# Performance work log

Hardware: AMD Instinct MI355X
Metric: run time of the kernel (lower is better)

## Reference

```python
import jax, jax.numpy as jnp
import numpy as np

DIM = 8          # per-head dim
EPS = 1e-15
GROUPS_PW = 192  # 3 * heads = 3 * 64


def _conv(x, w, groups=1, pad=0):
    return jax.lax.conv_general_dilated(
        x, w, window_strides=(1, 1), padding=[(pad, pad), (pad, pad)],
        dimension_numbers=('NCHW', 'OIHW', 'NCHW'), feature_group_count=groups)


def setup_inputs() -> dict:
    key = jax.random.key(0)
    k0, k1, k2, k3, k4 = jax.random.split(key, 5)
    B, C, H, W = 4, 512, 64, 64
    td = 512  # heads * dim
    x = jax.random.normal(k0, (B, C, H, W), jnp.float32)
    w_qkv = jax.random.normal(k1, (3 * td, C, 1, 1), jnp.float32) * 0.05
    w_dw = jax.random.normal(k2, (3 * td, 1, 5, 5), jnp.float32) * 0.05
    w_pw = jax.random.normal(k3, (3 * td, (3 * td) // GROUPS_PW, 1, 1), jnp.float32) * 0.05
    w_proj = jax.random.normal(k4, (C, 2 * td, 1, 1), jnp.float32) * 0.05
    return {'x': x, 'w_qkv': w_qkv, 'w_dw': w_dw, 'w_pw': w_pw, 'w_proj': w_proj}


def reference(x, w_qkv, w_dw, w_pw, w_proj):
    # qkv projection (1x1 conv, no bias, no norm/act per config)
    qkv = _conv(x, w_qkv)  # [B, 3*td, H, W]
    # multi-scale aggregation: depthwise 5x5 then grouped 1x1 (groups = 3*heads)
    agg = _conv(_conv(qkv, w_dw, groups=w_dw.shape[0], pad=2), w_pw, groups=GROUPS_PW)
    qkv = jnp.concatenate([qkv, agg], axis=1)  # [B, 6*td, H, W]

    B, _, H, W = qkv.shape
    qkv = qkv.reshape(B, -1, 3 * DIM, H * W)  # [B, h_eff, 3*dim, HW]
    q = jax.nn.relu(qkv[:, :, :DIM])          # [B, h, dim, HW]
    k = jax.nn.relu(qkv[:, :, DIM:2 * DIM])   # [B, h, dim, HW]
    v = qkv[:, :, 2 * DIM:]                   # [B, h, dim, HW]
    # pad v with a row of ones -> normalization trick
    v = jnp.pad(v, ((0, 0), (0, 0), (0, 1), (0, 0)), constant_values=1.0)
    # linear attention via associativity: (v k^T) q
    vk = jnp.einsum('bhdn,bhen->bhde', v, k)   # [B, h, dim+1, dim]
    out = jnp.einsum('bhde,bhen->bhdn', vk, q) # [B, h, dim+1, HW]
    out = out[:, :, :-1] / (out[:, :, -1:] + EPS)
    out = out.reshape(B, -1, H, W)             # [B, 2*td, H, W]
    return x + _conv(out, w_proj)
```

## Files before the change

kernel.cpp:

```cpp
#include <hip/hip_runtime.h>
#include <hip/hip_bf16.h>
#include <cstdint>
#include <cstddef>


typedef __hip_bfloat16 bf16;
typedef __attribute__((ext_vector_type(8))) short short8;
typedef __attribute__((ext_vector_type(4))) float f32x4;

__device__ __forceinline__ float b2f(bf16 v) { return __bfloat162float(v); }
__device__ __forceinline__ bf16 f2b(float v) { return __float2bfloat16(v); }

__device__ __forceinline__ void async16(void* lds_base, const void* gaddr) {
    __builtin_amdgcn_global_load_lds(
        (const __attribute__((address_space(1))) unsigned int*)gaddr,
        (__attribute__((address_space(3))) unsigned int*)lds_base,
        16, 0, 0);
}

__global__ __launch_bounds__(256) void convert_kernel(
    const float* __restrict__ src, bf16* __restrict__ dst, int n)
{
    int i = blockIdx.x * 256 + threadIdx.x;
    if (i < n) dst[i] = f2b(src[i]);
}

__global__ __launch_bounds__(256) void transpose_x_kernel(
    const float* __restrict__ x, bf16* __restrict__ x_t)
{
    __shared__ bf16 tile[32][33];
    const int b = blockIdx.z;
    const int c0 = blockIdx.y * 32;
    const int n0 = blockIdx.x * 32;
    const int tx = threadIdx.x & 31, ty = threadIdx.x >> 5;
    #pragma unroll
    for (int i = 0; i < 32; i += 8)
        tile[ty + i][tx] = f2b(x[((size_t)b * 512 + c0 + ty + i) * 4096 + n0 + tx]);
    __syncthreads();
    #pragma unroll
    for (int i = 0; i < 32; i += 8)
        x_t[((size_t)b * 4096 + n0 + ty + i) * 512 + c0 + tx] = tile[tx][ty + i];
}

template <bool PROJ>
__global__ __launch_bounds__(256) void mfma_gemm_kernel(
    const bf16* __restrict__ A, const bf16* __restrict__ xt_or_qkv,
    const bf16* __restrict__ agg, const float* __restrict__ X,
    void* __restrict__ Cout, int M, int K)
{
    constexpr int N = 4096;
    const int b = blockIdx.z;
    const int m_blk = blockIdx.y * 128;
    const int n_blk = blockIdx.x * 128;

    __shared__ short As[128 * 32];
    __shared__ short Bs[128 * 32];

    const int tid = threadIdx.x;
    const int lane = tid & 63, wave = tid >> 6;
    const int wm = (wave >> 1) * 64, wn = (wave & 1) * 64;
    const int fm = lane & 15, fq = lane >> 4;

    f32x4 acc[4][4] = {};

    const short* Ag = (const short*)A;
    const short* Btg = PROJ ? nullptr
        : (const short*)(xt_or_qkv + (size_t)b * N * 512);

    for (int k0 = 0; k0 < K; k0 += 32) {
        #pragma unroll
        for (int t0 = 0; t0 < 2; ++t0) {
            int t = wave + t0 * 4;
            int row = m_blk + t * 16 + (lane >> 2);
            int col = k0 + (lane & 3) * 8;
            async16(&As[t * 512], Ag + (size_t)row * K + col);
        }
        #pragma unroll
        for (int t0 = 0; t0 < 2; ++t0) {
            int t = wave + t0 * 4;
            int n = n_blk + t * 16 + (lane >> 2);
            if (!PROJ) {
                int col = k0 + (lane & 3) * 8;
                async16(&Bs[t * 512], Btg + (size_t)n * 512 + col);
            } else {
                int h = (k0 >> 3) + (lane & 3);
                const bf16* chunk = (h < 64 ? xt_or_qkv : agg) +
                    ((size_t)b * 1536 + (size_t)(h & 63) * 24 + 16) * 4096;
                async16(&Bs[t * 512], chunk + (size_t)n * 8);
            }
        }
        __syncthreads();

        short8 af[4], bfv[4];
        #pragma unroll
        for (int i = 0; i < 4; ++i)
            af[i] = *(const short8*)&As[(wm + i * 16 + fm) * 32 + fq * 8];
        #pragma unroll
        for (int j = 0; j < 4; ++j)
            bfv[j] = *(const short8*)&Bs[(wn + j * 16 + fm) * 32 + fq * 8];
        #pragma unroll
        for (int i = 0; i < 4; ++i)
            #pragma unroll
            for (int j = 0; j < 4; ++j)
                acc[i][j] = __builtin_amdgcn_mfma_f32_16x16x32_bf16(
                    af[i], bfv[j], acc[i][j], 0, 0, 0);
        __syncthreads();
    }

    if (!PROJ) {
        bf16* Cb = (bf16*)Cout + (size_t)b * M * N;
        #pragma unroll
        for (int i = 0; i < 4; ++i)
            #pragma unroll
            for (int j = 0; j < 4; ++j) {
                int n = n_blk + wn + j * 16 + fm;
                #pragma unroll
                for (int r = 0; r < 4; ++r) {
                    int m = m_blk + wm + i * 16 + fq * 4 + r;
                    Cb[(size_t)m * N + n] = f2b(acc[i][j][r]);
                }
            }
    } else {
        float* Ob = (float*)Cout + (size_t)b * M * N;
        const float* Xb = X + (size_t)b * M * N;
        #pragma unroll
        for (int i = 0; i < 4; ++i)
            #pragma unroll
            for (int j = 0; j < 4; ++j) {
                int n = n_blk + wn + j * 16 + fm;
                #pragma unroll
                for (int r = 0; r < 4; ++r) {
                    int m = m_blk + wm + i * 16 + fq * 4 + r;
                    size_t off = (size_t)m * N + n;
                    Ob[off] = acc[i][j][r] + Xb[off];
                }
            }
    }
}

__global__ __launch_bounds__(256) void dwpw_kernel(
    const bf16* __restrict__ qkv, const float* __restrict__ w_dw,
    const float* __restrict__ w_pw, bf16* __restrict__ agg)
{
    const int bg = blockIdx.y;
    const int b = bg / 192;
    const int g = bg - b * 192;
    const int y0 = blockIdx.x * 32;

    __shared__ float s_wdw[8][28];
    __shared__ float s_wpw[8][8];

    const int tid = threadIdx.x;

    if (tid < 200) {
        int c = tid / 25, k = tid - c * 25;
        s_wdw[c][k] = w_dw[(size_t)(g * 8 + c) * 25 + k];
    }
    if (tid < 64)
        s_wpw[tid >> 3][tid & 7] = w_pw[(size_t)(g * 8 + (tid >> 3)) * 8 + (tid & 7)];
    __syncthreads();

    const int py = tid >> 3;
    const int sx = tid & 7;
    const int yq = y0 + py;
    const size_t chan_base = ((size_t)b * 1536 + g * 8) * 4096;

    const int lo_off = (sx > 0) ? 16 * sx - 4 : 0;
    const int hi_off = (sx < 7) ? 16 * sx + 16 : 0;
    const unsigned lo_keep = (sx > 0) ? 0xFFFFFFFFu : 0u;
    const unsigned hi_keep = (sx < 7) ? 0xFFFFFFFFu : 0u;

    float dwv[8][8];
    #pragma unroll
    for (int c = 0; c < 8; ++c) {
        float w[25];
        #pragma unroll
        for (int q = 0; q < 6; ++q)
            *(float4*)&w[q * 4] = *(const float4*)&s_wdw[c][q * 4];
        w[24] = s_wdw[c][24];

        const char* cbase = (const char*)(qkv + chan_base + (size_t)c * 4096);
        float a[8] = {};
        #pragma unroll
        for (int i = 0; i < 5; ++i) {
            const int y = yq + i - 2;
            const bool row_ok = ((unsigned)y < 64u);
            const int yc = row_ok ? y : 0;
            const char* rowp = cbase + yc * 128;
            uint4 mid = *(const uint4*)(rowp + 16 * sx);
            unsigned lo = *(const unsigned*)(rowp + lo_off);
            unsigned hi = *(const unsigned*)(rowp + hi_off);
            const unsigned m = row_ok ? 0xFFFFFFFFu : 0u;
            lo &= m & lo_keep;
            hi &= m & hi_keep;
            mid.x &= m; mid.y &= m; mid.z &= m; mid.w &= m;

            float f[12];
            f[0]  = __uint_as_float(lo << 16);
            f[1]  = __uint_as_float(lo & 0xFFFF0000u);
            f[2]  = __uint_as_float(mid.x << 16);
            f[3]  = __uint_as_float(mid.x & 0xFFFF0000u);
            f[4]  = __uint_as_float(mid.y << 16);
            f[5]  = __uint_as_float(mid.y & 0xFFFF0000u);
            f[6]  = __uint_as_float(mid.z << 16);
            f[7]  = __uint_as_float(mid.z & 0xFFFF0000u);
            f[8]  = __uint_as_float(mid.w << 16);
            f[9]  = __uint_as_float(mid.w & 0xFFFF0000u);
            f[10] = __uint_as_float(hi << 16);
            f[11] = __uint_as_float(hi & 0xFFFF0000u);

            #pragma unroll
            for (int j = 0; j < 5; ++j) {
                float wi = w[i * 5 + j];
                #pragma unroll
                for (int x = 0; x < 8; ++x) a[x] += f[j + x] * wi;
            }
        }
        #pragma unroll
        for (int x = 0; x < 8; ++x) dwv[c][x] = a[x];
    }

    const size_t out_pix = (size_t)yq * 64 + 8 * sx;
    #pragma unroll
    for (int o = 0; o < 8; ++o) {
        float wv[8];
        *(float4*)&wv[0] = *(const float4*)&s_wpw[o][0];
        *(float4*)&wv[4] = *(const float4*)&s_wpw[o][4];
        float s[8] = {};
        #pragma unroll
        for (int i = 0; i < 8; ++i)
            #pragma unroll
            for (int x = 0; x < 8; ++x) s[x] += dwv[i][x] * wv[i];
        union { bf16 hv[8]; uint4 u; } pk;
        #pragma unroll
        for (int x = 0; x < 8; ++x) pk.hv[x] = f2b(s[x]);
        *(uint4*)(agg + chan_base + (size_t)o * 4096 + out_pix) = pk.u;
    }
}

__global__ __launch_bounds__(256) void vk_kernel(
    const bf16* __restrict__ qkv, const bf16* __restrict__ agg,
    float* __restrict__ vk)
{
    const int bh = blockIdx.x;
    const int b = bh >> 7;
    const int h = bh & 127;
    const bf16* base = (h < 64)
        ? (qkv + ((size_t)b * 1536 + h * 24) * 4096)
        : (agg + ((size_t)b * 1536 + (h - 64) * 24) * 4096);

    const int tid = threadIdx.x;
    float acc[9][8] = {};

    for (int n = tid; n < 4096; n += 256) {
        float kv[8], vv[8];
        #pragma unroll
        for (int e = 0; e < 8; ++e) kv[e] = fmaxf(b2f(base[(size_t)(8 + e) * 4096 + n]), 0.f);
        #pragma unroll
        for (int d = 0; d < 8; ++d) vv[d] = b2f(base[(size_t)(16 + d) * 4096 + n]);
        #pragma unroll
        for (int d = 0; d < 8; ++d)
            #pragma unroll
            for (int e = 0; e < 8; ++e)
                acc[d][e] += vv[d] * kv[e];
        #pragma unroll
        for (int e = 0; e < 8; ++e) acc[8][e] += kv[e];
    }

    __shared__ float red[4][72];
    const int lane = tid & 63, wave = tid >> 6;
    #pragma unroll
    for (int d = 0; d < 9; ++d) {
        #pragma unroll
        for (int e = 0; e < 8; ++e) {
            float v = acc[d][e];
            #pragma unroll
            for (int off = 32; off > 0; off >>= 1) v += __shfl_down(v, off, 64);
            if (lane == 0) red[wave][d * 8 + e] = v;
        }
    }
    __syncthreads();
    if (tid < 72) {
        float v = red[0][tid] + red[1][tid] + red[2][tid] + red[3][tid];
        vk[(size_t)bh * 72 + tid] = v;
    }
}

__global__ __launch_bounds__(256) void attn_out_kernel(
    bf16* __restrict__ qkv, bf16* __restrict__ agg,
    const float* __restrict__ vk)
{
    const int b = blockIdx.z;
    const int h = blockIdx.y;
    const int n = blockIdx.x * 256 + threadIdx.x;
    bf16* base = (h < 64)
        ? (qkv + ((size_t)b * 1536 + h * 24) * 4096)
        : (agg + ((size_t)b * 1536 + (h - 64) * 24) * 4096);

    __shared__ float s_vk[72];
    if (threadIdx.x < 72)
        s_vk[threadIdx.x] = vk[((size_t)b * 128 + h) * 72 + threadIdx.x];
    __syncthreads();

    float q[8];
    #pragma unroll
    for (int e = 0; e < 8; ++e) q[e] = fmaxf(b2f(base[(size_t)e * 4096 + n]), 0.f);

    float o[9];
    #pragma unroll
    for (int d = 0; d < 9; ++d) {
        float s = 0.f;
        #pragma unroll
        for (int e = 0; e < 8; ++e) s += s_vk[d * 8 + e] * q[e];
        o[d] = s;
    }
    const float denom = o[8] + 1e-15f;

    union { bf16 hv[8]; uint4 u; } pk;
    #pragma unroll
    for (int d = 0; d < 8; ++d) pk.hv[d] = f2b(o[d] / denom);
    *(uint4*)((char*)(base + (size_t)16 * 4096) + (size_t)n * 16) = pk.u;
}

extern "C" void kernel_launch(void* const* d_in, const int* in_sizes, int n_in,
                              void* d_out, int out_size, void* d_ws, size_t ws_size,
                              hipStream_t stream) {
    const float* x      = (const float*)d_in[0];
    const float* w_qkv  = (const float*)d_in[1];
    const float* w_dw   = (const float*)d_in[2];
    const float* w_pw   = (const float*)d_in[3];
    const float* w_proj = (const float*)d_in[4];

    char* ws = (char*)d_ws;
    bf16* w_qkv_bf  = (bf16*)ws;
    bf16* w_proj_bf = (bf16*)(ws + 1572864);
    float* vkbf     = (float*)(ws + 1572864 + 1048576);
    bf16* x_t       = (bf16*)(ws + 1572864 + 1048576 + 147456);
    bf16* qkv       = x_t + (size_t)4 * 4096 * 512;
    bf16* agg       = qkv + (size_t)4 * 1536 * 4096;

    convert_kernel<<<3072, 256, 0, stream>>>(w_qkv, w_qkv_bf, 786432);
    convert_kernel<<<2048, 256, 0, stream>>>(w_proj, w_proj_bf, 524288);
    transpose_x_kernel<<<dim3(128, 16, 4), 256, 0, stream>>>(x, x_t);

    mfma_gemm_kernel<false><<<dim3(32, 12, 4), 256, 0, stream>>>(
        w_qkv_bf, x_t, nullptr, nullptr, qkv, 1536, 512);

    dwpw_kernel<<<dim3(2, 768), 256, 0, stream>>>(qkv, w_dw, w_pw, agg);

    vk_kernel<<<dim3(512), 256, 0, stream>>>(qkv, agg, vkbf);

    attn_out_kernel<<<dim3(16, 128, 4), 256, 0, stream>>>(qkv, agg, vkbf);

    mfma_gemm_kernel<true><<<dim3(32, 4, 4), 256, 0, stream>>>(
        w_proj_bf, qkv, agg, x, d_out, 512, 1024);
}
```

Baseline: 263.8 us.

## Use bf16 dot2 for depthwise conv and vectorize vk/attn-out loads

The depthwise 5x5 conv now packs weights as bf16 pairs and uses the fdot2 bf16 instruction with alignbit-shifted pixel pairs instead of unpacking to fp32 FMAs. The vk and attn_out kernels switch from scalar bf16 loads to 16-byte short8 vector loads, with each thread handling 8 consecutive pixels (vk uses 512 threads covering all 4096 pixels in one pass). These target ALU overhead in the conv and memory-instruction count in the attention kernels. Depthwise weights are now rounded to bf16, which lowers precision slightly.

```diff
diff --git a/kernel.cpp b/kernel.cpp
--- a/kernel.cpp
+++ b/kernel.cpp
@@ -10,6 +10,22 @@
 
 __device__ __forceinline__ float b2f(bf16 v) { return __bfloat162float(v); }
 __device__ __forceinline__ bf16 f2b(float v) { return __float2bfloat16(v); }
+__device__ __forceinline__ float us2f(unsigned short u) {
+    return __uint_as_float(((unsigned)u) << 16);
+}
+
+__device__ __forceinline__ float dot2bf(unsigned p, unsigned wp, float acc) {
+#if __has_builtin(__builtin_amdgcn_fdot2_f32_bf16)
+    typedef __attribute__((ext_vector_type(2))) __bf16 bf16x2;
+    return __builtin_amdgcn_fdot2_f32_bf16(
+        __builtin_bit_cast(bf16x2, p), __builtin_bit_cast(bf16x2, wp),
+        acc, false);
+#else
+    return acc
+        + us2f((unsigned short)(p & 0xffffu))  * us2f((unsigned short)(wp & 0xffffu))
+        + us2f((unsigned short)(p >> 16))      * us2f((unsigned short)(wp >> 16));
+#endif
+}
 
 __device__ __forceinline__ void async16(void* lds_base, const void* gaddr) {
     __builtin_amdgcn_global_load_lds(
@@ -147,14 +163,20 @@
     const int g = bg - b * 192;
     const int y0 = blockIdx.x * 32;
 
-    __shared__ float s_wdw[8][28];
+    __shared__ unsigned s_wdwp[8][16];
     __shared__ float s_wpw[8][8];
 
     const int tid = threadIdx.x;
 
-    if (tid < 200) {
-        int c = tid / 25, k = tid - c * 25;
-        s_wdw[c][k] = w_dw[(size_t)(g * 8 + c) * 25 + k];
+    if (tid < 120) {
+        int c = tid / 15, s = tid - c * 15;
+        int i = s / 3, p = s - i * 3;
+        int idx = i * 5 + p * 2;
+        float w0 = w_dw[(size_t)(g * 8 + c) * 25 + idx];
+        float w1 = (p < 2) ? w_dw[(size_t)(g * 8 + c) * 25 + idx + 1] : 0.f;
+        unsigned u0 = __builtin_bit_cast(unsigned short, f2b(w0));
+        unsigned u1 = __builtin_bit_cast(unsigned short, f2b(w1));
+        s_wdwp[c][s] = u0 | (u1 << 16);
     }
     if (tid < 64)
         s_wpw[tid >> 3][tid & 7] = w_pw[(size_t)(g * 8 + (tid >> 3)) * 8 + (tid & 7)];
@@ -173,11 +195,10 @@
     float dwv[8][8];
     #pragma unroll
     for (int c = 0; c < 8; ++c) {
-        float w[25];
-        #pragma unroll
-        for (int q = 0; q < 6; ++q)
-            *(float4*)&w[q * 4] = *(const float4*)&s_wdw[c][q * 4];
-        w[24] = s_wdw[c][24];
+        unsigned wpq[16];
+        #pragma unroll
+        for (int q = 0; q < 4; ++q)
+            *(uint4*)&wpq[q * 4] = *(const uint4*)&s_wdwp[c][q * 4];
 
         const char* cbase = (const char*)(qkv + chan_base + (size_t)c * 4096);
         float a[8] = {};
@@ -191,30 +212,27 @@
             unsigned lo = *(const unsigned*)(rowp + lo_off);
             unsigned hi = *(const unsigned*)(rowp + hi_off);
             const unsigned m = row_ok ? 0xFFFFFFFFu : 0u;
-            lo &= m & lo_keep;
-            hi &= m & hi_keep;
-            mid.x &= m; mid.y &= m; mid.z &= m; mid.w &= m;
-
-            float f[12];
-            f[0]  = __uint_as_float(lo << 16);
-            f[1]  = __uint_as_float(lo & 0xFFFF0000u);
-            f[2]  = __uint_as_float(mid.x << 16);
-            f[3]  = __uint_as_float(mid.x & 0xFFFF0000u);
-            f[4]  = __uint_as_float(mid.y << 16);
-            f[5]  = __uint_as_float(mid.y & 0xFFFF0000u);
-            f[6]  = __uint_as_float(mid.z << 16);
-            f[7]  = __uint_as_float(mid.z & 0xFFFF0000u);
-            f[8]  = __uint_as_float(mid.w << 16);
-            f[9]  = __uint_as_float(mid.w & 0xFFFF0000u);
-            f[10] = __uint_as_float(hi << 16);
-            f[11] = __uint_as_float(hi & 0xFFFF0000u);
-
-            #pragma unroll
-            for (int j = 0; j < 5; ++j) {
-                float wi = w[i * 5 + j];
-                #pragma unroll
-                for (int x = 0; x < 8; ++x) a[x] += f[j + x] * wi;
-            }
+
+            unsigned W0 = lo & m & lo_keep;
+            unsigned W1 = mid.x & m, W2 = mid.y & m;
+            unsigned W3 = mid.z & m, W4 = mid.w & m;
+            unsigned W5 = hi & m & hi_keep;
+            unsigned S0 = __builtin_amdgcn_alignbit(W1, W0, 16);
+            unsigned S1 = __builtin_amdgcn_alignbit(W2, W1, 16);
+            unsigned S2 = __builtin_amdgcn_alignbit(W3, W2, 16);
+            unsigned S3 = __builtin_amdgcn_alignbit(W4, W3, 16);
+            unsigned S4 = __builtin_amdgcn_alignbit(W5, W4, 16);
+            unsigned S5 = W5 >> 16;
+
+            unsigned w01 = wpq[i * 3], w23 = wpq[i * 3 + 1], w4z = wpq[i * 3 + 2];
+            a[0] = dot2bf(W0, w01, dot2bf(W1, w23, dot2bf(W2, w4z, a[0])));
+            a[2] = dot2bf(W1, w01, dot2bf(W2, w23, dot2bf(W3, w4z, a[2])));
+            a[4] = dot2bf(W2, w01, dot2bf(W3, w23, dot2bf(W4, w4z, a[4])));
+            a[6] = dot2bf(W3, w01, dot2bf(W4, w23, dot2bf(W5, w4z, a[6])));
+            a[1] = dot2bf(S0, w01, dot2bf(S1, w23, dot2bf(S2, w4z, a[1])));
+            a[3] = dot2bf(S1, w01, dot2bf(S2, w23, dot2bf(S3, w4z, a[3])));
+            a[5] = dot2bf(S2, w01, dot2bf(S3, w23, dot2bf(S4, w4z, a[5])));
+            a[7] = dot2bf(S3, w01, dot2bf(S4, w23, dot2bf(S5, w4z, a[7])));
         }
         #pragma unroll
         for (int x = 0; x < 8; ++x) dwv[c][x] = a[x];
@@ -238,7 +256,7 @@
     }
 }
 
-__global__ __launch_bounds__(256) void vk_kernel(
+__global__ __launch_bounds__(512) void vk_kernel(
     const bf16* __restrict__ qkv, const bf16* __restrict__ agg,
     float* __restrict__ vk)
 {
@@ -250,24 +268,36 @@
         : (agg + ((size_t)b * 1536 + (h - 64) * 24) * 4096);
 
     const int tid = threadIdx.x;
+    const int n0 = tid * 8;
+
+    short8 kr[8], vr[8];
+    #pragma unroll
+    for (int e = 0; e < 8; ++e)
+        kr[e] = *(const short8*)&base[(size_t)(8 + e) * 4096 + n0];
+    #pragma unroll
+    for (int d = 0; d < 8; ++d)
+        vr[d] = *(const short8*)&base[(size_t)(16 + d) * 4096 + n0];
+
     float acc[9][8] = {};
-
-    for (int n = tid; n < 4096; n += 256) {
-        float kv[8], vv[8];
-        #pragma unroll
-        for (int e = 0; e < 8; ++e) kv[e] = fmaxf(b2f(base[(size_t)(8 + e) * 4096 + n]), 0.f);
-        #pragma unroll
-        for (int d = 0; d < 8; ++d) vv[d] = b2f(base[(size_t)(16 + d) * 4096 + n]);
+    #pragma unroll
+    for (int t = 0; t < 8; ++t) {
+        float kt[8], vt[8];
+        #pragma unroll
+        for (int e = 0; e < 8; ++e)
+            kt[e] = fmaxf(us2f((unsigned short)kr[e][t]), 0.f);
         #pragma unroll
         for (int d = 0; d < 8; ++d)
+            vt[d] = us2f((unsigned short)vr[d][t]);
+        #pragma unroll
+        for (int d = 0; d < 8; ++d)
             #pragma unroll
             for (int e = 0; e < 8; ++e)
-                acc[d][e] += vv[d] * kv[e];
-        #pragma unroll
-        for (int e = 0; e < 8; ++e) acc[8][e] += kv[e];
-    }
-
-    __shared__ float red[4][72];
+                acc[d][e] += vt[d] * kt[e];
+        #pragma unroll
+        for (int e = 0; e < 8; ++e) acc[8][e] += kt[e];
+    }
+
+    __shared__ float red[8][72];
     const int lane = tid & 63, wave = tid >> 6;
     #pragma unroll
     for (int d = 0; d < 9; ++d) {
@@ -281,7 +311,9 @@
     }
     __syncthreads();
     if (tid < 72) {
-        float v = red[0][tid] + red[1][tid] + red[2][tid] + red[3][tid];
+        float v = 0.f;
+        #pragma unroll
+        for (int w = 0; w < 8; ++w) v += red[w][tid];
         vk[(size_t)bh * 72 + tid] = v;
     }
 }
@@ -292,7 +324,7 @@
 {
     const int b = blockIdx.z;
     const int h = blockIdx.y;
-    const int n = blockIdx.x * 256 + threadIdx.x;
+    const int n0 = (blockIdx.x * 256 + threadIdx.x) * 8;
     bf16* base = (h < 64)
         ? (qkv + ((size_t)b * 1536 + h * 24) * 4096)
         : (agg + ((size_t)b * 1536 + (h - 64) * 24) * 4096);
@@ -302,24 +334,34 @@
         s_vk[threadIdx.x] = vk[((size_t)b * 128 + h) * 72 + threadIdx.x];
     __syncthreads();
 
-    float q[8];
-    #pragma unroll
-    for (int e = 0; e < 8; ++e) q[e] = fmaxf(b2f(base[(size_t)e * 4096 + n]), 0.f);
-
-    float o[9];
-    #pragma unroll
-    for (int d = 0; d < 9; ++d) {
-        float s = 0.f;
-        #pragma unroll
-        for (int e = 0; e < 8; ++e) s += s_vk[d * 8 + e] * q[e];
-        o[d] = s;
-    }
-    const float denom = o[8] + 1e-15f;
-
-    union { bf16 hv[8]; uint4 u; } pk;
-    #pragma unroll
-    for (int d = 0; d < 8; ++d) pk.hv[d] = f2b(o[d] / denom);
-    *(uint4*)((char*)(base + (size_t)16 * 4096) + (size_t)n * 16) = pk.u;
+    short8 qr[8];
+    #pragma unroll
+    for (int e = 0; e < 8; ++e)
+        qr[e] = *(const short8*)&base[(size_t)e * 4096 + n0];
+
+    char* outp = (char*)(base + (size_t)16 * 4096) + (size_t)n0 * 16;
+    #pragma unroll
+    for (int t = 0; t < 8; ++t) {
+        float q[8];
+        #pragma unroll
+        for (int e = 0; e < 8; ++e)
+            q[e] = fmaxf(us2f((unsigned short)qr[e][t]), 0.f);
+
+        float o[9];
+        #pragma unroll
+        for (int d = 0; d < 9; ++d) {
+            float s = 0.f;
+            #pragma unroll
+            for (int e = 0; e < 8; ++e) s += s_vk[d * 8 + e] * q[e];
+            o[d] = s;
+        }
+        const float denom = o[8] + 1e-15f;
+
+        union { bf16 hv[8]; uint4 u; } pk;
+        #pragma unroll
+        for (int d = 0; d < 8; ++d) pk.hv[d] = f2b(o[d] / denom);
+        *(uint4*)(outp + (size_t)t * 16) = pk.u;
+    }
 }
 
 extern "C" void kernel_launch(void* const* d_in, const int* in_sizes, int n_in,
@@ -348,9 +390,9 @@
 
     dwpw_kernel<<<dim3(2, 768), 256, 0, stream>>>(qkv, w_dw, w_pw, agg);
 
-    vk_kernel<<<dim3(512), 256, 0, stream>>>(qkv, agg, vkbf);
-
-    attn_out_kernel<<<dim3(16, 128, 4), 256, 0, stream>>>(qkv, agg, vkbf);
+    vk_kernel<<<dim3(512), 512, 0, stream>>>(qkv, agg, vkbf);
+
+    attn_out_kernel<<<dim3(2, 128, 4), 256, 0, stream>>>(qkv, agg, vkbf);
 
     mfma_gemm_kernel<true><<<dim3(32, 4, 4), 256, 0, stream>>>(
         w_proj_bf, qkv, agg, x, d_out, 512, 1024);
```

After: 269.7 us. 1.02x slower.
